# Kernel optimization log

Measured on AMD Instinct MI355X. Metric: run time of the kernel, lower is better.

## Reference

```python
import jax, jax.numpy as jnp
import numpy as np

GAMMA = 0.99
STEP_TYPE_LAST = 2  # alf.data_structures.StepType.LAST
T, B = 256, 65536


def setup_inputs() -> dict:
    key = jax.random.key(0)
    k = jax.random.split(key, 7)
    return {
        "reward": jax.random.normal(k[0], (T, B), dtype=jnp.float32),
        "discount": jax.random.uniform(k[1], (T, B), dtype=jnp.float32),
        "value": jax.random.normal(k[2], (T, B), dtype=jnp.float32),
        "target_value": jax.random.normal(k[3], (T, B), dtype=jnp.float32),
        "step_type": jax.random.randint(k[4], (T, B), 0, 3, dtype=jnp.int32),
        "rollout_b": jax.random.randint(k[5], (T, B), 0, 2, dtype=jnp.int32),
        "train_b": jax.random.randint(k[6], (T, B), 0, 2, dtype=jnp.int32),
    }


def _discounted_return(rewards, values, is_lasts, discounts):
    # Backward recursion:
    #   rets[T-1] = values[T-1]; acc[T-1] = values[T-1]
    #   rets[t] = acc[t+1] * discounts[t+1] + rewards[t+1]
    #   acc[t]  = is_lasts[t] * values[t] + (1 - is_lasts[t]) * rets[t]
    # returns rets[0:T-1]  (shape [T-1, B])
    il = is_lasts.astype(values.dtype)
    xs = (discounts[1:], rewards[1:], il[:-1], values[:-1])
    xs_rev = jax.tree_util.tree_map(lambda x: x[::-1], xs)  # scan t = T-2 .. 0

    def step(acc, x):
        d, r, l, v = x
        ret = acc * d + r
        acc_new = l * v + (1.0 - l) * ret
        return acc_new, ret

    _, rets_rev = jax.lax.scan(step, values[-1], xs_rev)
    return jax.lax.stop_gradient(rets_rev[::-1])  # [T-1, B]


def reference(reward, discount, value, target_value, step_type, rollout_b, train_b):
    discounts = discount * GAMMA
    b = (rollout_b != 0) | (train_b != 0)
    b = b.at[0].set(False)
    is_lasts = (step_type == STEP_TYPE_LAST) | b
    returns = _discounted_return(reward, target_value, is_lasts, discounts)
    v = value[:-1]
    loss = jnp.square(returns - v)                 # element_wise_squared_loss
    loss = jnp.concatenate([loss, jnp.zeros_like(loss[:1])], axis=0)  # extend zero -> [T, B]
    return loss
```

## Files before the change

### kernel.cpp

```cpp
#include <hip/hip_runtime.h>

#define T_STEPS 256
#define B_COLS  65536u
#define GAMMA_F 0.99f

#define CHUNK   16
#define NCHUNK  (T_STEPS / CHUNK)
#define BCOL    32

__global__ __launch_bounds__(512, 4) void td_loss_kernel(
    const float* __restrict__ reward,
    const float* __restrict__ discount,
    const float* __restrict__ value,
    const float* __restrict__ target_value,
    const int*   __restrict__ step_type,
    const int*   __restrict__ rollout_b,
    const int*   __restrict__ train_b,
    float*       __restrict__ out)
{
    const int x  = threadIdx.x;
    const int ch = threadIdx.y;
    const unsigned col  = blockIdx.x * BCOL + x;
    const int      hi   = ch * CHUNK + (CHUNK - 1);
    const unsigned base = (unsigned)hi * B_COLS + col;

    __shared__ float s_alpha[NCHUNK][BCOL];
    __shared__ float s_beta [NCHUNK][BCOL];
    __shared__ float s_accin[NCHUNK][BCOL];

    unsigned mask = 0;
#pragma unroll
    for (int j = 0; j < CHUNK; ++j)
        mask |= (unsigned)(step_type[base - (unsigned)j * B_COLS] == 2) << j;
#pragma unroll
    for (int j = 0; j < CHUNK; ++j)
        mask |= (unsigned)(rollout_b[base - (unsigned)j * B_COLS] != 0) << j;
#pragma unroll
    for (int j = 0; j < CHUNK; ++j)
        mask |= (unsigned)(train_b[base - (unsigned)j * B_COLS] != 0) << j;
    if (ch == NCHUNK - 1) mask |= 1u;

    float D[CHUNK], r[CHUNK], tv[CHUNK], v[CHUNK];
#pragma unroll
    for (int j = 0; j < CHUNK; ++j) {
        const unsigned idx  = base - (unsigned)j * B_COLS;
        const unsigned idx1 = (hi - j == T_STEPS - 1) ? idx : idx + B_COLS;
        D[j]  = discount[idx1] * GAMMA_F;
        r[j]  = reward[idx1];
        tv[j] = target_value[idx];
        v[j]  = value[idx];
    }

    float alpha = 1.0f, beta = 0.0f;
#pragma unroll
    for (int j = 0; j < CHUNK; ++j) {
        const bool  l = (mask >> j) & 1u;
        const float g = l ? 0.0f : D[j];
        const float o = l ? tv[j] : r[j];
        beta  = fmaf(g, beta, o);
        alpha *= g;
    }
    s_alpha[ch][x] = alpha;
    s_beta [ch][x] = beta;
    __syncthreads();

    if (ch == 0) {
        float acc = 0.0f;
#pragma unroll
        for (int k = NCHUNK - 1; k >= 0; --k) {
            s_accin[k][x] = acc;
            acc = fmaf(s_alpha[k][x], acc, s_beta[k][x]);
        }
    }
    __syncthreads();

    float acc = s_accin[ch][x];
#pragma unroll
    for (int j = 0; j < CHUNK; ++j) {
        const float ret  = fmaf(acc, D[j], r[j]);
        const bool  l    = (mask >> j) & 1u;
        acc = l ? tv[j] : ret;
        const float diff = ret - v[j];
        float o = diff * diff;
        if (hi - j == T_STEPS - 1) o = 0.0f;
        out[base - (unsigned)j * B_COLS] = o;
    }
}

extern "C" void kernel_launch(void* const* d_in, const int* in_sizes, int n_in,
                              void* d_out, int out_size, void* d_ws, size_t ws_size,
                              hipStream_t stream) {
    const float* reward       = (const float*)d_in[0];
    const float* discount     = (const float*)d_in[1];
    const float* value        = (const float*)d_in[2];
    const float* target_value = (const float*)d_in[3];
    const int*   step_type    = (const int*)d_in[4];
    const int*   rollout_b    = (const int*)d_in[5];
    const int*   train_b      = (const int*)d_in[6];
    float*       out          = (float*)d_out;

    dim3 block(BCOL, NCHUNK);
    dim3 grid(B_COLS / BCOL);
    td_loss_kernel<<<grid, block, 0, stream>>>(
        reward, discount, value, target_value, step_type, rollout_b, train_b, out);
}
```

Before: 424.9 us.

## Vectorize column loads to float4 and re-read inputs instead of holding registers

Each thread now handles four adjacent columns using 128-bit int4/float4 loads and stores, which widens memory transactions and cuts the grid by four. To keep register pressure manageable, the pass-one data is loaded in halves and discarded. The second pass reloads discount, reward and target_value from global memory rather than keeping them in registers. This trades roughly a third more global reads, likely served from cache, for wider accesses and fewer loads issued.

```diff
diff --git a/kernel.cpp b/kernel.cpp
--- a/kernel.cpp
+++ b/kernel.cpp
@@ -6,7 +6,9 @@
 
 #define CHUNK   16
 #define NCHUNK  (T_STEPS / CHUNK)
-#define BCOL    32
+#define XT      32
+#define CPT     4
+#define BLKCOLS (XT * CPT)
 
 __global__ __launch_bounds__(512, 4) void td_loss_kernel(
     const float* __restrict__ reward,
@@ -20,70 +22,129 @@
 {
     const int x  = threadIdx.x;
     const int ch = threadIdx.y;
-    const unsigned col  = blockIdx.x * BCOL + x;
+    const unsigned col  = (blockIdx.x * XT + x) * CPT;
     const int      hi   = ch * CHUNK + (CHUNK - 1);
     const unsigned base = (unsigned)hi * B_COLS + col;
 
-    __shared__ float s_alpha[NCHUNK][BCOL];
-    __shared__ float s_beta [NCHUNK][BCOL];
-    __shared__ float s_accin[NCHUNK][BCOL];
+    __shared__ float4 s_alpha[NCHUNK][XT];
+    __shared__ float4 s_beta [NCHUNK][XT];
+    __shared__ float4 s_accin[NCHUNK][XT];
 
-    unsigned mask = 0;
-#pragma unroll
-    for (int j = 0; j < CHUNK; ++j)
-        mask |= (unsigned)(step_type[base - (unsigned)j * B_COLS] == 2) << j;
-#pragma unroll
-    for (int j = 0; j < CHUNK; ++j)
-        mask |= (unsigned)(rollout_b[base - (unsigned)j * B_COLS] != 0) << j;
-#pragma unroll
-    for (int j = 0; j < CHUNK; ++j)
-        mask |= (unsigned)(train_b[base - (unsigned)j * B_COLS] != 0) << j;
-    if (ch == NCHUNK - 1) mask |= 1u;
-
-    float D[CHUNK], r[CHUNK], tv[CHUNK], v[CHUNK];
+    unsigned msk[4] = {0u, 0u, 0u, 0u};
 #pragma unroll
     for (int j = 0; j < CHUNK; ++j) {
-        const unsigned idx  = base - (unsigned)j * B_COLS;
-        const unsigned idx1 = (hi - j == T_STEPS - 1) ? idx : idx + B_COLS;
-        D[j]  = discount[idx1] * GAMMA_F;
-        r[j]  = reward[idx1];
-        tv[j] = target_value[idx];
-        v[j]  = value[idx];
+        const int4 s = *reinterpret_cast<const int4*>(step_type + (base - (unsigned)j * B_COLS));
+        msk[0] |= (unsigned)(s.x == 2) << j;
+        msk[1] |= (unsigned)(s.y == 2) << j;
+        msk[2] |= (unsigned)(s.z == 2) << j;
+        msk[3] |= (unsigned)(s.w == 2) << j;
     }
-
-    float alpha = 1.0f, beta = 0.0f;
 #pragma unroll
     for (int j = 0; j < CHUNK; ++j) {
-        const bool  l = (mask >> j) & 1u;
-        const float g = l ? 0.0f : D[j];
-        const float o = l ? tv[j] : r[j];
-        beta  = fmaf(g, beta, o);
-        alpha *= g;
+        const int4 s = *reinterpret_cast<const int4*>(rollout_b + (base - (unsigned)j * B_COLS));
+        msk[0] |= (unsigned)(s.x != 0) << j;
+        msk[1] |= (unsigned)(s.y != 0) << j;
+        msk[2] |= (unsigned)(s.z != 0) << j;
+        msk[3] |= (unsigned)(s.w != 0) << j;
     }
-    s_alpha[ch][x] = alpha;
-    s_beta [ch][x] = beta;
+#pragma unroll
+    for (int j = 0; j < CHUNK; ++j) {
+        const int4 s = *reinterpret_cast<const int4*>(train_b + (base - (unsigned)j * B_COLS));
+        msk[0] |= (unsigned)(s.x != 0) << j;
+        msk[1] |= (unsigned)(s.y != 0) << j;
+        msk[2] |= (unsigned)(s.z != 0) << j;
+        msk[3] |= (unsigned)(s.w != 0) << j;
+    }
+    if (ch == NCHUNK - 1) { msk[0] |= 1u; msk[1] |= 1u; msk[2] |= 1u; msk[3] |= 1u; }
+
+    float al[4] = {1.f, 1.f, 1.f, 1.f};
+    float be[4] = {0.f, 0.f, 0.f, 0.f};
+#pragma unroll
+    for (int h = 0; h < 2; ++h) {
+        float4 D[8], R[8], TV[8];
+#pragma unroll
+        for (int jj = 0; jj < 8; ++jj) {
+            const int j = h * 8 + jj;
+            const unsigned idx  = base - (unsigned)j * B_COLS;
+            const unsigned idx1 = (hi - j == T_STEPS - 1) ? idx : idx + B_COLS;
+            float4 d = *reinterpret_cast<const float4*>(discount + idx1);
+            d.x *= GAMMA_F; d.y *= GAMMA_F; d.z *= GAMMA_F; d.w *= GAMMA_F;
+            D[jj]  = d;
+            R[jj]  = *reinterpret_cast<const float4*>(reward + idx1);
+            TV[jj] = *reinterpret_cast<const float4*>(target_value + idx);
+        }
+#pragma unroll
+        for (int jj = 0; jj < 8; ++jj) {
+            const int j = h * 8 + jj;
+            const float* Dv = reinterpret_cast<const float*>(&D[jj]);
+            const float* Rv = reinterpret_cast<const float*>(&R[jj]);
+            const float* Tv = reinterpret_cast<const float*>(&TV[jj]);
+#pragma unroll
+            for (int k = 0; k < 4; ++k) {
+                const bool  l = (msk[k] >> j) & 1u;
+                const float g = l ? 0.0f : Dv[k];
+                const float o = l ? Tv[k] : Rv[k];
+                be[k] = fmaf(g, be[k], o);
+                al[k] *= g;
+            }
+        }
+    }
+    s_alpha[ch][x] = make_float4(al[0], al[1], al[2], al[3]);
+    s_beta [ch][x] = make_float4(be[0], be[1], be[2], be[3]);
     __syncthreads();
 
     if (ch == 0) {
-        float acc = 0.0f;
+        float a0 = 0.f, a1 = 0.f, a2 = 0.f, a3 = 0.f;
 #pragma unroll
         for (int k = NCHUNK - 1; k >= 0; --k) {
-            s_accin[k][x] = acc;
-            acc = fmaf(s_alpha[k][x], acc, s_beta[k][x]);
+            s_accin[k][x] = make_float4(a0, a1, a2, a3);
+            const float4 A  = s_alpha[k][x];
+            const float4 Bv = s_beta [k][x];
+            a0 = fmaf(A.x, a0, Bv.x);
+            a1 = fmaf(A.y, a1, Bv.y);
+            a2 = fmaf(A.z, a2, Bv.z);
+            a3 = fmaf(A.w, a3, Bv.w);
         }
     }
     __syncthreads();
 
-    float acc = s_accin[ch][x];
+    const float4 a0v = s_accin[ch][x];
+    float ac[4] = {a0v.x, a0v.y, a0v.z, a0v.w};
 #pragma unroll
-    for (int j = 0; j < CHUNK; ++j) {
-        const float ret  = fmaf(acc, D[j], r[j]);
-        const bool  l    = (mask >> j) & 1u;
-        acc = l ? tv[j] : ret;
-        const float diff = ret - v[j];
-        float o = diff * diff;
-        if (hi - j == T_STEPS - 1) o = 0.0f;
-        out[base - (unsigned)j * B_COLS] = o;
+    for (int q = 0; q < 4; ++q) {
+        float4 D[4], R[4], TV[4], V[4];
+#pragma unroll
+        for (int jj = 0; jj < 4; ++jj) {
+            const int j = q * 4 + jj;
+            const unsigned idx  = base - (unsigned)j * B_COLS;
+            const unsigned idx1 = (hi - j == T_STEPS - 1) ? idx : idx + B_COLS;
+            float4 d = *reinterpret_cast<const float4*>(discount + idx1);
+            d.x *= GAMMA_F; d.y *= GAMMA_F; d.z *= GAMMA_F; d.w *= GAMMA_F;
+            D[jj]  = d;
+            R[jj]  = *reinterpret_cast<const float4*>(reward + idx1);
+            TV[jj] = *reinterpret_cast<const float4*>(target_value + idx);
+            V[jj]  = *reinterpret_cast<const float4*>(value + idx);
+        }
+#pragma unroll
+        for (int jj = 0; jj < 4; ++jj) {
+            const int j = q * 4 + jj;
+            const float* Dv = reinterpret_cast<const float*>(&D[jj]);
+            const float* Rv = reinterpret_cast<const float*>(&R[jj]);
+            const float* Tv = reinterpret_cast<const float*>(&TV[jj]);
+            const float* Vv = reinterpret_cast<const float*>(&V[jj]);
+            float o[4];
+#pragma unroll
+            for (int k = 0; k < 4; ++k) {
+                const float ret  = fmaf(ac[k], Dv[k], Rv[k]);
+                const bool  l    = (msk[k] >> j) & 1u;
+                ac[k] = l ? Tv[k] : ret;
+                const float diff = ret - Vv[k];
+                o[k] = diff * diff;
+            }
+            float4 ov = make_float4(o[0], o[1], o[2], o[3]);
+            if (hi - j == T_STEPS - 1) ov = make_float4(0.f, 0.f, 0.f, 0.f);
+            *reinterpret_cast<float4*>(out + (base - (unsigned)j * B_COLS)) = ov;
+        }
     }
 }
 
@@ -99,8 +160,8 @@
     const int*   train_b      = (const int*)d_in[6];
     float*       out          = (float*)d_out;
 
-    dim3 block(BCOL, NCHUNK);
-    dim3 grid(B_COLS / BCOL);
+    dim3 block(XT, NCHUNK);
+    dim3 grid(B_COLS / BLKCOLS);
     td_loss_kernel<<<grid, block, 0, stream>>>(
         reward, discount, value, target_value, step_type, rollout_b, train_b, out);
 }
```

Result: slower. 504.6 us (+18.8%).
